# Kernel tuning notes

Measured on AMD Instinct MI355X. Metric: run time of the kernel, lower is better.

The kernel has to match this reference:

```python
import jax, jax.numpy as jnp
import numpy as np

TIM_SIZE, TIM_EMB = 48, 64
APP_SIZE, APP_EMB = 10000, 256
UID_SIZE, UID_EMB = 10000, 256
INPUT_SIZE = TIM_EMB + APP_EMB  # 320
S = 4096
N = S - 3  # windows of length 4


def setup_inputs() -> dict:
    key = jax.random.key(0)
    ks = jax.random.split(key, 12)
    inp = {
        "tim": jax.random.randint(ks[0], (S, 1), 0, TIM_SIZE),
        "app": jax.random.uniform(ks[1], (S, APP_SIZE), dtype=jnp.float32),
        "loc": jax.random.randint(ks[2], (S, 1), 0, 1),
        "uid": jax.random.randint(ks[3], (1,), 0, UID_SIZE),
        "ptim": jax.random.randint(ks[4], (N, 1), 0, TIM_SIZE),
        # learned parameters
        "emb_tim_w": jax.random.normal(ks[5], (TIM_SIZE, TIM_EMB), dtype=jnp.float32) * 0.02,
        "emb_uid_w": jax.random.normal(ks[6], (UID_SIZE, UID_EMB), dtype=jnp.float32) * 0.02,
        "emb_app_w": jax.random.normal(ks[7], (APP_SIZE, APP_EMB), dtype=jnp.float32) * 0.02,
        "attn_W": jax.random.uniform(ks[8], (INPUT_SIZE, 1), dtype=jnp.float32),
        "attn_b": jax.random.uniform(ks[9], (4, 1), dtype=jnp.float32),
        "attn_fc_w": jax.random.normal(ks[10], (APP_EMB, INPUT_SIZE), dtype=jnp.float32) * 0.02,
        "attn_fc_b": jnp.zeros((APP_EMB,), dtype=jnp.float32),
        "dec_w": jax.random.normal(ks[11], (APP_SIZE, APP_EMB + TIM_EMB), dtype=jnp.float32) * 0.02,
        "dec_b": jnp.zeros((APP_SIZE,), dtype=jnp.float32),
    }
    return inp


def reference(tim, app, loc, uid, ptim, emb_tim_w, emb_uid_w, emb_app_w,
              attn_W, attn_b, attn_fc_w, attn_fc_b, dec_w, dec_b):
    # embeddings (squeeze(1) in torch)
    tim_emb = emb_tim_w[tim[:, 0]]    # [S, TIM_EMB]
    ptim_emb = emb_tim_w[ptim[:, 0]]  # [N, TIM_EMB]
    # 'sum' app embedding mode: multi-hot @ table
    app_emb = app @ emb_app_w         # [S, APP_EMB]
    x = jnp.concatenate([app_emb, tim_emb], axis=1)  # [S, INPUT_SIZE]; dropout is identity at eval
    # sliding windows of length 4 (vectorizes the torch per-i loop)
    n = tim.shape[0] - 3
    idx = jnp.arange(n)[:, None] + jnp.arange(4)[None, :]  # [N, 4]
    win = x[idx]                                          # [N, 4, INPUT_SIZE]
    H = jnp.tanh(win @ attn_W + attn_b)                   # [N, 4, 1]
    Xn = H / jnp.sum(jnp.abs(H), axis=(1, 2), keepdims=True)  # L1 normalize over the window
    pooled = jnp.einsum('nf,nfd->nd', Xn[:, :, 0], win)   # [N, INPUT_SIZE]
    out = pooled @ attn_fc_w.T + attn_fc_b                # [N, APP_EMB]
    uid_emb = emb_uid_w[uid[0]]                           # [APP_EMB], broadcast = repeat
    out = out * uid_emb
    out = jnp.concatenate([out, ptim_emb], axis=1)        # [N, APP_EMB+TIM_EMB]
    score = jax.nn.sigmoid(out @ dec_w.T + dec_b)         # [N, APP_SIZE]
    return score
```

## Files before the change

kernel.cpp:

```cpp
#include <hip/hip_runtime.h>

typedef __attribute__((ext_vector_type(8))) short  bf16x8;
typedef __attribute__((ext_vector_type(8))) unsigned short u16x8;
typedef __attribute__((ext_vector_type(4))) float  f32x4;

constexpr int S    = 4096;
constexpr int NR   = 4093;
constexpr int KAPP = 10000;
constexpr int EAPP = 256;
constexpr int ETIM = 64;
constexpr int DIN  = 320;
constexpr int NDEC = 10000;
constexpr int NSK  = 8;
constexpr int KCH  = 1280;
constexpr int KPAD = NSK * KCH;
constexpr int NS   = KCH / 32;

__device__ inline unsigned short f2bf(float f) {
    unsigned u = __float_as_uint(f);
    u += 0x7fffu + ((u >> 16) & 1u);
    return (unsigned short)(u >> 16);
}
__device__ inline float bf2f(unsigned short h) {
    return __uint_as_float(((unsigned)h) << 16);
}
__device__ inline u16x8 pack8(f32x4 a, f32x4 b) {
    u16x8 v;
    v[0]=f2bf(a.x); v[1]=f2bf(a.y); v[2]=f2bf(a.z); v[3]=f2bf(a.w);
    v[4]=f2bf(b.x); v[5]=f2bf(b.y); v[6]=f2bf(b.z); v[7]=f2bf(b.w);
    return v;
}
__device__ inline bf16x8 as_bf(u16x8 v) {
    union { u16x8 u; bf16x8 b; } c; c.u = v; return c.b;
}

__global__ __launch_bounds__(256) void k_cvt_bf16(
    const float* __restrict__ in, unsigned short* __restrict__ out, int n8)
{
    int id = blockIdx.x * 256 + threadIdx.x;
    if (id >= n8) return;
    const float* p = in + (size_t)id * 8;
    f32x4 a = *reinterpret_cast<const f32x4*>(p);
    f32x4 b = *reinterpret_cast<const f32x4*>(p + 4);
    *reinterpret_cast<u16x8*>(out + (size_t)id * 8) = pack8(a, b);
}

__global__ __launch_bounds__(256) void k_transpose_appw(
    const float* __restrict__ B, unsigned short* __restrict__ Bp)
{
    __shared__ float T[64][68];
    const int kt = blockIdx.x * 64, nt = blockIdx.y * 64;
    const int tid = threadIdx.x;
    #pragma unroll
    for (int i = 0; i < 4; ++i) {
        int c = tid + (i << 8);
        int k = c >> 4, n4 = (c & 15) << 2;
        f32x4 v = {0.f, 0.f, 0.f, 0.f};
        if (kt + k < KAPP)
            v = *reinterpret_cast<const f32x4*>(&B[(size_t)(kt + k) * EAPP + nt + n4]);
        *reinterpret_cast<f32x4*>(&T[k][n4]) = v;
    }
    __syncthreads();
    #pragma unroll
    for (int i = 0; i < 2; ++i) {
        int c = tid + (i << 8);
        int n = c >> 3, ko = (c & 7) << 3;
        u16x8 v;
        #pragma unroll
        for (int j = 0; j < 8; ++j) v[j] = f2bf(T[ko + j][n]);
        *reinterpret_cast<u16x8*>(&Bp[(size_t)(nt + n) * KPAD + kt + ko]) = v;
    }
}

__global__ __launch_bounds__(256) void k_embed_tim(
    const int* __restrict__ tim, const float* __restrict__ emb_tim,
    unsigned short* __restrict__ xb)
{
    int r = blockIdx.x * 4 + (threadIdx.x >> 6);
    int e = threadIdx.x & 63;
    xb[(size_t)r * DIN + EAPP + e] = f2bf(emb_tim[tim[r] * ETIM + e]);
}
__global__ __launch_bounds__(256) void k_embed_ptim(
    const int* __restrict__ ptim, const float* __restrict__ emb_tim,
    unsigned short* __restrict__ yb)
{
    int r = blockIdx.x * 4 + (threadIdx.x >> 6);
    int e = threadIdx.x & 63;
    if (r < NR) yb[(size_t)r * DIN + EAPP + e] = f2bf(emb_tim[ptim[r] * ETIM + e]);
}

__global__ __launch_bounds__(256, 4) void k_app(
    const float* __restrict__ A, const unsigned short* __restrict__ Bp,
    float* __restrict__ part)
{
    __shared__ unsigned short As[2][4 * 32 * 8];
    __shared__ unsigned short Bs[2][4 * 256 * 8];
    const int tid = threadIdx.x, lane = tid & 63, w = tid >> 6;
    const int ks = blockIdx.x, bm = blockIdx.y << 5;
    const int wc = w << 6, rl = lane & 15, kq = lane >> 4;
    const int k0 = ks * KCH;
    const int arow = tid >> 2, ac = tid & 3;

    u16x8 ra, rb[4];
    auto gload = [&](int step) {
        const int kt = k0 + (step << 5);
        if (tid < 128) {
            const int k = kt + (ac << 3);
            u16x8 v = {0,0,0,0,0,0,0,0};
            if (k < KAPP) {
                const float* p = &A[(size_t)(bm + arow) * KAPP + k];
                v = pack8(*reinterpret_cast<const f32x4*>(p),
                          *reinterpret_cast<const f32x4*>(p + 4));
            }
            ra = v;
        }
        #pragma unroll
        for (int i = 0; i < 4; ++i) {
            int c = tid + (i << 8);
            int row = c >> 2, ck = c & 3;
            rb[i] = *reinterpret_cast<const u16x8*>(
                &Bp[(size_t)row * KPAD + kt + (ck << 3)]);
        }
    };
    auto swrite = [&](int b) {
        if (tid < 128)
            *reinterpret_cast<u16x8*>(&As[b][((ac << 5) + arow) << 3]) = ra;
        #pragma unroll
        for (int i = 0; i < 4; ++i) {
            int c = tid + (i << 8);
            int row = c >> 2, ck = c & 3;
            *reinterpret_cast<u16x8*>(&Bs[b][((ck << 8) + row) << 3]) = rb[i];
        }
    };

    f32x4 acc[2][4];
    #pragma unroll
    for (int i = 0; i < 2; ++i)
        #pragma unroll
        for (int j = 0; j < 4; ++j) acc[i][j] = (f32x4){0.f, 0.f, 0.f, 0.f};

    gload(0); swrite(0); __syncthreads();
    for (int t = 0; t < NS; ++t) {
        const int cur = t & 1;
        const bool more = (t + 1 < NS);
        if (more) gload(t + 1);
        bf16x8 af[2], bfr[4];
        #pragma unroll
        for (int i = 0; i < 2; ++i)
            af[i] = *reinterpret_cast<const bf16x8*>(
                &As[cur][((kq << 5) + i * 16 + rl) << 3]);
        #pragma unroll
        for (int j = 0; j < 4; ++j)
            bfr[j] = *reinterpret_cast<const bf16x8*>(
                &Bs[cur][((kq << 8) + wc + j * 16 + rl) << 3]);
        #pragma unroll
        for (int i = 0; i < 2; ++i)
            #pragma unroll
            for (int j = 0; j < 4; ++j)
                acc[i][j] = __builtin_amdgcn_mfma_f32_16x16x32_bf16(
                    af[i], bfr[j], acc[i][j], 0, 0, 0);
        if (more) swrite(cur ^ 1);
        __syncthreads();
    }

    float* P = part + ((size_t)ks * S + bm) * EAPP;
    const int rq = kq << 2;
    #pragma unroll
    for (int i = 0; i < 2; ++i)
        #pragma unroll
        for (int j = 0; j < 4; ++j) {
            int col = wc + j * 16 + rl;
            #pragma unroll
            for (int q = 0; q < 4; ++q)
                __builtin_nontemporal_store(acc[i][j][q],
                    &P[(size_t)(i * 16 + rq + q) * EAPP + col]);
        }
}

__global__ __launch_bounds__(256) void k_reduce_app(
    const float* __restrict__ part, unsigned short* __restrict__ xb)
{
    int id = blockIdx.x * 256 + threadIdx.x;
    int row = id >> 6, c4 = (id & 63) << 2;
    f32x4 s = {0.f, 0.f, 0.f, 0.f};
    #pragma unroll
    for (int sl = 0; sl < NSK; ++sl) {
        f32x4 v = __builtin_nontemporal_load(reinterpret_cast<const f32x4*>(
            &part[((size_t)sl * S + row) * EAPP + c4]));
        s.x += v.x; s.y += v.y; s.z += v.z; s.w += v.w;
    }
    unsigned short* o = &xb[(size_t)row * DIN + c4];
    o[0] = f2bf(s.x); o[1] = f2bf(s.y); o[2] = f2bf(s.z); o[3] = f2bf(s.w);
}

__global__ __launch_bounds__(256) void k_score(
    const unsigned short* __restrict__ xb, const float* __restrict__ W,
    float* __restrict__ s)
{
    int wv = threadIdx.x >> 6, lane = threadIdx.x & 63;
    int m = blockIdx.x * 4 + wv;
    float sum = 0.f;
    #pragma unroll
    for (int i = 0; i < 5; ++i) {
        int k = lane + (i << 6);
        sum += bf2f(xb[(size_t)m * DIN + k]) * W[k];
    }
    #pragma unroll
    for (int off = 32; off; off >>= 1) sum += __shfl_down(sum, off);
    if (lane == 0) s[m] = sum;
}

__global__ void k_pooled(
    const unsigned short* __restrict__ xb, const float* __restrict__ s,
    const float* __restrict__ attn_b, unsigned short* __restrict__ pooledb)
{
    int n = blockIdx.x, d = threadIdx.x;
    float h[4], den = 0.f;
    #pragma unroll
    for (int f = 0; f < 4; ++f) {
        h[f] = tanhf(s[n + f] + attn_b[f]);
        den += fabsf(h[f]);
    }
    float inv = 1.f / den, p = 0.f;
    #pragma unroll
    for (int f = 0; f < 4; ++f)
        p = fmaf(h[f] * inv, bf2f(xb[(size_t)(n + f) * DIN + d]), p);
    pooledb[(size_t)n * DIN + d] = f2bf(p);
}

template<int EPI>
__global__ __launch_bounds__(256, 4) void k_nt320(
    const unsigned short* __restrict__ A, const unsigned short* __restrict__ B,
    int Nb, int Mlim,
    const float* __restrict__ bias,
    const float* __restrict__ emb_uid, const int* __restrict__ uid,
    void* __restrict__ Cout, int ldc)
{
    __shared__ unsigned short As[40 * 64 * 8];
    const int tid = threadIdx.x, lane = tid & 63, w = tid >> 6;
    const int qx = gridDim.x >> 3;
    const int swz = (blockIdx.x & 7) * qx + (blockIdx.x >> 3);
    const int nbn = (Nb + 255) >> 8;
    const int bm = (swz / nbn) << 6, bn = (swz % nbn) << 8;
    const int rl = lane & 15, kq = lane >> 4;
    const int wc = w << 6;

    {
        const int row = tid >> 2, c0 = tid & 3;
        const unsigned short* src = A + (size_t)(bm + row) * DIN;
        #pragma unroll
        for (int t = 0; t < 10; ++t) {
            int ck = c0 + (t << 2);
            *reinterpret_cast<u16x8*>(&As[((ck << 6) + row) << 3]) =
                *reinterpret_cast<const u16x8*>(src + (ck << 3));
        }
    }
    __syncthreads();

    f32x4 acc[4][4];
    #pragma unroll
    for (int i = 0; i < 4; ++i)
        #pragma unroll
        for (int j = 0; j < 4; ++j) acc[i][j] = (f32x4){0.f, 0.f, 0.f, 0.f};

    u16x8 b0[4], b1[4];
#define LOADB(DST, KSN) do {                                                    \
    const int kg_ = ((KSN) << 5) + (kq << 3);                                   \
    _Pragma("unroll")                                                           \
    for (int j = 0; j < 4; ++j) {                                               \
        int brow = bn + wc + j * 16 + rl;                                       \
        u16x8 v_ = {0,0,0,0,0,0,0,0};                                           \
        if (brow < Nb)                                                          \
            v_ = *reinterpret_cast<const u16x8*>(&B[(size_t)brow * DIN + kg_]); \
        DST[j] = v_;                                                            \
    }                                                                           \
} while (0)

#define STEPNT(BARR, KSN) do {                                                  \
    const int ckb_ = (((KSN) << 2) + kq) << 6;                                  \
    bf16x8 af_[4];                                                              \
    _Pragma("unroll")                                                           \
    for (int i = 0; i < 4; ++i)                                                 \
        af_[i] = *reinterpret_cast<const bf16x8*>(                              \
            &As[(ckb_ + i * 16 + rl) << 3]);                                    \
    _Pragma("unroll")                                                           \
    for (int i = 0; i < 4; ++i)                                                 \
        _Pragma("unroll")                                                       \
        for (int j = 0; j < 4; ++j)                                             \
            acc[i][j] = __builtin_amdgcn_mfma_f32_16x16x32_bf16(                \
                af_[i], as_bf(BARR[j]), acc[i][j], 0, 0, 0);                     \
} while (0)

    LOADB(b0, 0);
    LOADB(b1, 1);
    #pragma unroll
    for (int p = 0; p < 5; ++p) {
        STEPNT(b0, 2 * p);
        if (2 * p + 2 < 10) LOADB(b0, 2 * p + 2);
        STEPNT(b1, 2 * p + 1);
        if (2 * p + 3 < 10) LOADB(b1, 2 * p + 3);
    }
#undef LOADB
#undef STEPNT

    const int rq = kq << 2;
    if (EPI == 1) {
        unsigned short* C = (unsigned short*)Cout;
        const float* us = emb_uid + (size_t)uid[0] * EAPP;
        #pragma unroll
        for (int j = 0; j < 4; ++j) {
            int col = bn + wc + j * 16 + rl;
            if (col >= Nb) continue;
            float um = us[col], bb = bias[col];
            #pragma unroll
            for (int i = 0; i < 4; ++i)
                #pragma unroll
                for (int q = 0; q < 4; ++q) {
                    int row = bm + i * 16 + rq + q;
                    if (row < Mlim)
                        C[(size_t)row * ldc + col] = f2bf((acc[i][j][q] + bb) * um);
                }
        }
    } else {
        float* C = (float*)Cout;
        float* epi = reinterpret_cast<float*>(As);
        float bb[4];
        #pragma unroll
        for (int j = 0; j < 4; ++j) {
            int col = bn + wc + j * 16 + rl;
            bb[j] = (col < Nb) ? bias[col] : 0.f;
        }
        const int r16 = tid >> 6, c4 = (tid & 63) << 2;
        #pragma unroll
        for (int i = 0; i < 4; ++i) {
            __syncthreads();
            #pragma unroll
            for (int j = 0; j < 4; ++j) {
                int colL = wc + j * 16 + rl;
                #pragma unroll
                for (int q = 0; q < 4; ++q) {
                    float v = acc[i][j][q] + bb[j];
                    epi[(rq + q) * 260 + colL] = 1.f / (1.f + __expf(-v));
                }
            }
            __syncthreads();
            #pragma unroll
            for (int r4 = 0; r4 < 4; ++r4) {
                int rowL = (r4 << 2) + r16;
                int grow = bm + (i << 4) + rowL;
                f32x4 v = *reinterpret_cast<const f32x4*>(&epi[rowL * 260 + c4]);
                if (grow < Mlim) {
                    if (bn + 256 <= Nb) {
                        __builtin_nontemporal_store(v,
                            reinterpret_cast<f32x4*>(&C[(size_t)grow * ldc + bn + c4]));
                    } else {
                        #pragma unroll
                        for (int e = 0; e < 4; ++e)
                            if (bn + c4 + e < Nb)
                                __builtin_nontemporal_store(v[e],
                                    &C[(size_t)grow * ldc + bn + c4 + e]);
                    }
                }
            }
        }
    }
}

extern "C" void kernel_launch(void* const* d_in, const int* in_sizes, int n_in,
                              void* d_out, int out_size, void* d_ws, size_t ws_size,
                              hipStream_t stream)
{
    const int*   tim       = (const int*)  d_in[0];
    const float* app       = (const float*)d_in[1];
    const int*   uid       = (const int*)  d_in[3];
    const int*   ptim      = (const int*)  d_in[4];
    const float* emb_tim_w = (const float*)d_in[5];
    const float* emb_uid_w = (const float*)d_in[6];
    const float* emb_app_w = (const float*)d_in[7];
    const float* attn_W    = (const float*)d_in[8];
    const float* attn_b    = (const float*)d_in[9];
    const float* attn_fc_w = (const float*)d_in[10];
    const float* attn_fc_b = (const float*)d_in[11];
    const float* dec_w     = (const float*)d_in[12];
    const float* dec_b     = (const float*)d_in[13];
    float* out = (float*)d_out;

    char* w = (char*)d_ws;
    size_t o = 0;
    auto alloc = [&](size_t bytes) { char* p = w + o; o = (o + bytes + 511) & ~(size_t)511; return p; };
    unsigned short* xb      = (unsigned short*)alloc((size_t)S * DIN * 2);
    unsigned short* pooledb = (unsigned short*)alloc((size_t)S * DIN * 2);
    unsigned short* yb      = (unsigned short*)alloc((size_t)S * DIN * 2);
    float*          s       = (float*)        alloc((size_t)S * 4);
    unsigned short* Bp      = (unsigned short*)alloc((size_t)EAPP * KPAD * 2);
    unsigned short* decb    = (unsigned short*)alloc((size_t)NDEC * DIN * 2);
    unsigned short* fcb     = (unsigned short*)alloc((size_t)EAPP * DIN * 2);
    float*          part    = (float*)        alloc((size_t)NSK * S * EAPP * 4);

    k_cvt_bf16<<<(NDEC * DIN / 8 + 255) / 256, 256, 0, stream>>>(dec_w, decb, NDEC * DIN / 8);
    k_cvt_bf16<<<(EAPP * DIN / 8 + 255) / 256, 256, 0, stream>>>(attn_fc_w, fcb, EAPP * DIN / 8);
    dim3 gT(KPAD / 64, EAPP / 64);
    k_transpose_appw<<<gT, 256, 0, stream>>>(emb_app_w, Bp);
    k_embed_tim<<<S / 4, 256, 0, stream>>>(tim, emb_tim_w, xb);

    dim3 gApp(NSK, S / 32);
    k_app<<<gApp, 256, 0, stream>>>(app, Bp, part);
    k_reduce_app<<<S * 64 / 256, 256, 0, stream>>>(part, xb);

    k_score<<<S / 4, 256, 0, stream>>>(xb, attn_W, s);
    k_pooled<<<NR, DIN, 0, stream>>>(xb, s, attn_b, pooledb);
    k_embed_ptim<<<S / 4, 256, 0, stream>>>(ptim, emb_tim_w, yb);

    k_nt320<1><<<64, 256, 0, stream>>>(pooledb, fcb, EAPP, S,
                                       attn_fc_b, emb_uid_w, uid, yb, DIN);
    k_nt320<2><<<40 * 64, 256, 0, stream>>>(yb, decb, NDEC, NR,
                                            dec_b, nullptr, nullptr, out, NDEC);
}
```

Before: 219.4 us.

## Pre-tile app weights and stream B via direct global-to-LDS loads

Rewrites the app-embedding weight preprocessing so the bf16 weights are stored in the exact per-step LDS tile order. The main GEMM then streams them with global_load_lds (direct to shared memory) instead of going through registers. The A operand (multi-hot fp32) is now loaded straight into registers in MFMA fragment order and converted there, which drops the A shared-memory tile. The loop is double-buffered with explicit waitcnt and barrier. This cuts register staging and LDS write traffic but serializes on vmcnt(0) each step, and A loads become less coalesced.

```diff
diff --git a/kernel.cpp b/kernel.cpp
--- a/kernel.cpp
+++ b/kernel.cpp
@@ -45,8 +45,8 @@
     *reinterpret_cast<u16x8*>(out + (size_t)id * 8) = pack8(a, b);
 }
 
-__global__ __launch_bounds__(256) void k_transpose_appw(
-    const float* __restrict__ B, unsigned short* __restrict__ Bp)
+__global__ __launch_bounds__(256) void k_bake_appw(
+    const float* __restrict__ B, unsigned short* __restrict__ Bpp)
 {
     __shared__ float T[64][68];
     const int kt = blockIdx.x * 64, nt = blockIdx.y * 64;
@@ -64,11 +64,13 @@
     #pragma unroll
     for (int i = 0; i < 2; ++i) {
         int c = tid + (i << 8);
-        int n = c >> 3, ko = (c & 7) << 3;
+        int ln = c & 63, lc = c >> 6;
+        int t = (kt >> 5) + (lc >> 2), ck = lc & 3;
         u16x8 v;
         #pragma unroll
-        for (int j = 0; j < 8; ++j) v[j] = f2bf(T[ko + j][n]);
-        *reinterpret_cast<u16x8*>(&Bp[(size_t)(nt + n) * KPAD + kt + ko]) = v;
+        for (int h = 0; h < 8; ++h) v[h] = f2bf(T[(lc << 3) + h][ln]);
+        *reinterpret_cast<u16x8*>(
+            &Bpp[((size_t)t * 1024 + (ck << 8) + nt + ln) * 8]) = v;
     }
 }
 
@@ -90,48 +92,16 @@
 }
 
 __global__ __launch_bounds__(256, 4) void k_app(
-    const float* __restrict__ A, const unsigned short* __restrict__ Bp,
+    const float* __restrict__ A, const unsigned short* __restrict__ Bpp,
     float* __restrict__ part)
 {
-    __shared__ unsigned short As[2][4 * 32 * 8];
-    __shared__ unsigned short Bs[2][4 * 256 * 8];
+    __shared__ unsigned short Bs[2][8192];
     const int tid = threadIdx.x, lane = tid & 63, w = tid >> 6;
     const int ks = blockIdx.x, bm = blockIdx.y << 5;
     const int wc = w << 6, rl = lane & 15, kq = lane >> 4;
-    const int k0 = ks * KCH;
-    const int arow = tid >> 2, ac = tid & 3;
-
-    u16x8 ra, rb[4];
-    auto gload = [&](int step) {
-        const int kt = k0 + (step << 5);
-        if (tid < 128) {
-            const int k = kt + (ac << 3);
-            u16x8 v = {0,0,0,0,0,0,0,0};
-            if (k < KAPP) {
-                const float* p = &A[(size_t)(bm + arow) * KAPP + k];
-                v = pack8(*reinterpret_cast<const f32x4*>(p),
-                          *reinterpret_cast<const f32x4*>(p + 4));
-            }
-            ra = v;
-        }
-        #pragma unroll
-        for (int i = 0; i < 4; ++i) {
-            int c = tid + (i << 8);
-            int row = c >> 2, ck = c & 3;
-            rb[i] = *reinterpret_cast<const u16x8*>(
-                &Bp[(size_t)row * KPAD + kt + (ck << 3)]);
-        }
-    };
-    auto swrite = [&](int b) {
-        if (tid < 128)
-            *reinterpret_cast<u16x8*>(&As[b][((ac << 5) + arow) << 3]) = ra;
-        #pragma unroll
-        for (int i = 0; i < 4; ++i) {
-            int c = tid + (i << 8);
-            int row = c >> 2, ck = c & 3;
-            *reinterpret_cast<u16x8*>(&Bs[b][((ck << 8) + row) << 3]) = rb[i];
-        }
-    };
+
+    const unsigned short* gB = Bpp + (size_t)(ks * NS) * 8192
+                                   + ((w << 2) << 9) + lane * 8;
 
     f32x4 acc[2][4];
     #pragma unroll
@@ -139,29 +109,62 @@
         #pragma unroll
         for (int j = 0; j < 4; ++j) acc[i][j] = (f32x4){0.f, 0.f, 0.f, 0.f};
 
-    gload(0); swrite(0); __syncthreads();
-    for (int t = 0; t < NS; ++t) {
-        const int cur = t & 1;
-        const bool more = (t + 1 < NS);
-        if (more) gload(t + 1);
-        bf16x8 af[2], bfr[4];
-        #pragma unroll
-        for (int i = 0; i < 2; ++i)
-            af[i] = *reinterpret_cast<const bf16x8*>(
-                &As[cur][((kq << 5) + i * 16 + rl) << 3]);
-        #pragma unroll
-        for (int j = 0; j < 4; ++j)
-            bfr[j] = *reinterpret_cast<const bf16x8*>(
-                &Bs[cur][((kq << 8) + wc + j * 16 + rl) << 3]);
-        #pragma unroll
-        for (int i = 0; i < 2; ++i)
-            #pragma unroll
-            for (int j = 0; j < 4; ++j)
-                acc[i][j] = __builtin_amdgcn_mfma_f32_16x16x32_bf16(
-                    af[i], bfr[j], acc[i][j], 0, 0, 0);
-        if (more) swrite(cur ^ 1);
-        __syncthreads();
-    }
+    f32x4 a0[2][2], a1[2][2];
+
+#define LOADA(T, DST) do {                                                      \
+    const int kg_ = ks * KCH + ((T) << 5) + (kq << 3);                          \
+    _Pragma("unroll")                                                           \
+    for (int i = 0; i < 2; ++i) {                                               \
+        f32x4 z_ = {0.f, 0.f, 0.f, 0.f};                                        \
+        DST[i][0] = z_; DST[i][1] = z_;                                         \
+        if (kg_ + 8 <= KAPP) {                                                  \
+            const float* p_ = &A[(size_t)(bm + (i << 4) + rl) * KAPP + kg_];    \
+            DST[i][0] = *reinterpret_cast<const f32x4*>(p_);                    \
+            DST[i][1] = *reinterpret_cast<const f32x4*>(p_ + 4);                \
+        }                                                                       \
+    }                                                                           \
+} while (0)
+
+#define STAGEB(T, BUF) do {                                                     \
+    const unsigned short* s_ = gB + (size_t)(T) * 8192;                         \
+    _Pragma("unroll")                                                           \
+    for (int q = 0; q < 4; ++q)                                                 \
+        __builtin_amdgcn_global_load_lds(                                       \
+            (const __attribute__((address_space(1))) void*)(s_ + (q << 9)),     \
+            (__attribute__((address_space(3))) void*)(                          \
+                &Bs[BUF][(((w << 2) + q) << 9)]),                               \
+            16, 0, 0);                                                          \
+} while (0)
+
+#define PHASE(T, CURA, NXTA, CURB) do {                                         \
+    asm volatile("s_waitcnt vmcnt(0)" ::: "memory");                            \
+    __builtin_amdgcn_s_barrier();                                               \
+    __builtin_amdgcn_sched_barrier(0);                                          \
+    if ((T) + 1 < NS) { STAGEB((T) + 1, 1 - (CURB)); LOADA((T) + 1, NXTA); }    \
+    bf16x8 af_[2], bf_[4];                                                      \
+    _Pragma("unroll")                                                           \
+    for (int i = 0; i < 2; ++i)                                                 \
+        af_[i] = as_bf(pack8(CURA[i][0], CURA[i][1]));                          \
+    _Pragma("unroll")                                                           \
+    for (int j = 0; j < 4; ++j)                                                 \
+        bf_[j] = *reinterpret_cast<const bf16x8*>(                              \
+            &Bs[CURB][((kq << 8) + wc + (j << 4) + rl) << 3]);                  \
+    _Pragma("unroll")                                                           \
+    for (int i = 0; i < 2; ++i)                                                 \
+        _Pragma("unroll")                                                       \
+        for (int j = 0; j < 4; ++j)                                             \
+            acc[i][j] = __builtin_amdgcn_mfma_f32_16x16x32_bf16(                \
+                af_[i], bf_[j], acc[i][j], 0, 0, 0);                            \
+} while (0)
+
+    LOADA(0, a0); STAGEB(0, 0);
+    for (int t2 = 0; t2 < NS; t2 += 2) {
+        PHASE(t2,     a0, a1, 0);
+        PHASE(t2 + 1, a1, a0, 1);
+    }
+#undef LOADA
+#undef STAGEB
+#undef PHASE
 
     float* P = part + ((size_t)ks * S + bm) * EAPP;
     const int rq = kq << 2;
@@ -392,7 +395,7 @@
     unsigned short* pooledb = (unsigned short*)alloc((size_t)S * DIN * 2);
     unsigned short* yb      = (unsigned short*)alloc((size_t)S * DIN * 2);
     float*          s       = (float*)        alloc((size_t)S * 4);
-    unsigned short* Bp      = (unsigned short*)alloc((size_t)EAPP * KPAD * 2);
+    unsigned short* Bpp     = (unsigned short*)alloc((size_t)EAPP * KPAD * 2);
     unsigned short* decb    = (unsigned short*)alloc((size_t)NDEC * DIN * 2);
     unsigned short* fcb     = (unsigned short*)alloc((size_t)EAPP * DIN * 2);
     float*          part    = (float*)        alloc((size_t)NSK * S * EAPP * 4);
@@ -400,11 +403,11 @@
     k_cvt_bf16<<<(NDEC * DIN / 8 + 255) / 256, 256, 0, stream>>>(dec_w, decb, NDEC * DIN / 8);
     k_cvt_bf16<<<(EAPP * DIN / 8 + 255) / 256, 256, 0, stream>>>(attn_fc_w, fcb, EAPP * DIN / 8);
     dim3 gT(KPAD / 64, EAPP / 64);
-    k_transpose_appw<<<gT, 256, 0, stream>>>(emb_app_w, Bp);
+    k_bake_appw<<<gT, 256, 0, stream>>>(emb_app_w, Bpp);
     k_embed_tim<<<S / 4, 256, 0, stream>>>(tim, emb_tim_w, xb);
 
     dim3 gApp(NSK, S / 32);
-    k_app<<<gApp, 256, 0, stream>>>(app, Bp, part);
+    k_app<<<gApp, 256, 0, stream>>>(app, Bpp, part);
     k_reduce_app<<<S * 64 / 256, 256, 0, stream>>>(part, xb);
 
     k_score<<<S / 4, 256, 0, stream>>>(xb, attn_W, s);
```

New measurement: 232.7 us. 1.06x slower.

## Stream B fragments directly from global into registers in app GEMM

Applied to the files above, without the earlier changes.

Restructures the app-embedding split-K GEMM so that each chunk of 320 K values of A is staged once into padded shared memory (row stride 41 to avoid bank conflicts), with one barrier pair per chunk instead of one per 32-wide step. The B operand is no longer staged through shared memory. Each lane loads its MFMA B fragments straight from global memory into registers, double-buffered across K steps. This removes most LDS traffic and barriers, at the cost of more per-lane global loads of B and less overlap of A loading with compute.

```diff
diff --git a/kernel.cpp b/kernel.cpp
--- a/kernel.cpp
+++ b/kernel.cpp
@@ -13,8 +13,9 @@
 constexpr int NDEC = 10000;
 constexpr int NSK  = 8;
 constexpr int KCH  = 1280;
-constexpr int KPAD = NSK * KCH;
-constexpr int NS   = KCH / 32;
+constexpr int CH   = 320;
+constexpr int NCH  = KCH / CH;
+constexpr int KPAD = 10240;
 
 __device__ inline unsigned short f2bf(float f) {
     unsigned u = __float_as_uint(f);
@@ -93,75 +94,76 @@
     const float* __restrict__ A, const unsigned short* __restrict__ Bp,
     float* __restrict__ part)
 {
-    __shared__ unsigned short As[2][4 * 32 * 8];
-    __shared__ unsigned short Bs[2][4 * 256 * 8];
+    __shared__ unsigned short As[32 * 41 * 8];
     const int tid = threadIdx.x, lane = tid & 63, w = tid >> 6;
     const int ks = blockIdx.x, bm = blockIdx.y << 5;
     const int wc = w << 6, rl = lane & 15, kq = lane >> 4;
-    const int k0 = ks * KCH;
-    const int arow = tid >> 2, ac = tid & 3;
-
-    u16x8 ra, rb[4];
-    auto gload = [&](int step) {
-        const int kt = k0 + (step << 5);
-        if (tid < 128) {
-            const int k = kt + (ac << 3);
-            u16x8 v = {0,0,0,0,0,0,0,0};
-            if (k < KAPP) {
-                const float* p = &A[(size_t)(bm + arow) * KAPP + k];
-                v = pack8(*reinterpret_cast<const f32x4*>(p),
-                          *reinterpret_cast<const f32x4*>(p + 4));
+
+    f32x4 acc[2][4];
+    #pragma unroll
+    for (int i = 0; i < 2; ++i)
+        #pragma unroll
+        for (int j = 0; j < 4; ++j) acc[i][j] = (f32x4){0.f, 0.f, 0.f, 0.f};
+
+    u16x8 b0[4], b1[4];
+
+#define LOADB(DST, KB, KSN) do {                                                \
+    const int kg_ = (KB) + ((KSN) << 5) + (kq << 3);                            \
+    _Pragma("unroll")                                                           \
+    for (int j = 0; j < 4; ++j) {                                               \
+        int brow = wc + j * 16 + rl;                                            \
+        DST[j] = *reinterpret_cast<const u16x8*>(                               \
+            &Bp[(size_t)brow * KPAD + kg_]);                                    \
+    }                                                                           \
+} while (0)
+
+#define STEP(BARR, KSN) do {                                                    \
+    const int ckb_ = ((KSN) << 2) + kq;                                         \
+    bf16x8 af_[2];                                                              \
+    _Pragma("unroll")                                                           \
+    for (int i = 0; i < 2; ++i)                                                 \
+        af_[i] = *reinterpret_cast<const bf16x8*>(                              \
+            &As[(((i << 4) + rl) * 41 + ckb_) << 3]);                           \
+    _Pragma("unroll")                                                           \
+    for (int i = 0; i < 2; ++i)                                                 \
+        _Pragma("unroll")                                                       \
+        for (int j = 0; j < 4; ++j)                                             \
+            acc[i][j] = __builtin_amdgcn_mfma_f32_16x16x32_bf16(                \
+                af_[i], as_bf(BARR[j]), acc[i][j], 0, 0, 0);                     \
+} while (0)
+
+    for (int c = 0; c < NCH; ++c) {
+        const int kb = ks * KCH + c * CH;
+        __syncthreads();
+        {
+            const int row = tid >> 3, c0 = tid & 7;
+            const float* src = A + (size_t)(bm + row) * KAPP + kb;
+            #pragma unroll
+            for (int t = 0; t < 5; ++t) {
+                int ck = c0 + (t << 3);
+                u16x8 v = {0,0,0,0,0,0,0,0};
+                if (kb + (ck << 3) + 8 <= KAPP) {
+                    const float* p = src + (ck << 3);
+                    v = pack8(*reinterpret_cast<const f32x4*>(p),
+                              *reinterpret_cast<const f32x4*>(p + 4));
+                }
+                *reinterpret_cast<u16x8*>(&As[(row * 41 + ck) << 3]) = v;
             }
-            ra = v;
-        }
-        #pragma unroll
-        for (int i = 0; i < 4; ++i) {
-            int c = tid + (i << 8);
-            int row = c >> 2, ck = c & 3;
-            rb[i] = *reinterpret_cast<const u16x8*>(
-                &Bp[(size_t)row * KPAD + kt + (ck << 3)]);
-        }
-    };
-    auto swrite = [&](int b) {
-        if (tid < 128)
-            *reinterpret_cast<u16x8*>(&As[b][((ac << 5) + arow) << 3]) = ra;
-        #pragma unroll
-        for (int i = 0; i < 4; ++i) {
-            int c = tid + (i << 8);
-            int row = c >> 2, ck = c & 3;
-            *reinterpret_cast<u16x8*>(&Bs[b][((ck << 8) + row) << 3]) = rb[i];
-        }
-    };
-
-    f32x4 acc[2][4];
-    #pragma unroll
-    for (int i = 0; i < 2; ++i)
-        #pragma unroll
-        for (int j = 0; j < 4; ++j) acc[i][j] = (f32x4){0.f, 0.f, 0.f, 0.f};
-
-    gload(0); swrite(0); __syncthreads();
-    for (int t = 0; t < NS; ++t) {
-        const int cur = t & 1;
-        const bool more = (t + 1 < NS);
-        if (more) gload(t + 1);
-        bf16x8 af[2], bfr[4];
-        #pragma unroll
-        for (int i = 0; i < 2; ++i)
-            af[i] = *reinterpret_cast<const bf16x8*>(
-                &As[cur][((kq << 5) + i * 16 + rl) << 3]);
-        #pragma unroll
-        for (int j = 0; j < 4; ++j)
-            bfr[j] = *reinterpret_cast<const bf16x8*>(
-                &Bs[cur][((kq << 8) + wc + j * 16 + rl) << 3]);
-        #pragma unroll
-        for (int i = 0; i < 2; ++i)
-            #pragma unroll
-            for (int j = 0; j < 4; ++j)
-                acc[i][j] = __builtin_amdgcn_mfma_f32_16x16x32_bf16(
-                    af[i], bfr[j], acc[i][j], 0, 0, 0);
-        if (more) swrite(cur ^ 1);
+        }
         __syncthreads();
-    }
+
+        LOADB(b0, kb, 0);
+        LOADB(b1, kb, 1);
+        #pragma unroll
+        for (int p = 0; p < 5; ++p) {
+            STEP(b0, 2 * p);
+            if (2 * p + 2 < 10) LOADB(b0, kb, 2 * p + 2);
+            STEP(b1, 2 * p + 1);
+            if (2 * p + 3 < 10) LOADB(b1, kb, 2 * p + 3);
+        }
+    }
+#undef LOADB
+#undef STEP
 
     float* P = part + ((size_t)ks * S + bm) * EAPP;
     const int rq = kq << 2;
```

Result: slower. 243.4 us (+11.0%).
